# Performance work log

Measured on AMD Instinct MI355X. Metric: run time of the kernel, lower is better.

The kernel has to match this reference:

```python
import jax, jax.numpy as jnp
import numpy as np


def setup_inputs() -> dict:
    key = jax.random.key(0)
    k1, k2, k3, k4, k5 = jax.random.split(key, 5)
    N, C, H, W, HID = 32, 3, 64, 64, 256
    x = jax.random.normal(k1, (N, C, H, W), dtype=jnp.float32)
    w_xh = jax.random.normal(k2, (HID, C), dtype=jnp.float32) * (1.0 / np.sqrt(C))
    b_xh = jax.random.normal(k3, (HID,), dtype=jnp.float32) * 0.02
    w_hh = jax.random.normal(k4, (HID, HID), dtype=jnp.float32) * (1.0 / np.sqrt(HID))
    b_hh = jax.random.normal(k5, (HID,), dtype=jnp.float32) * 0.02
    return {"x": x, "w_xh": w_xh, "b_xh": b_xh, "w_hh": w_hh, "b_hh": b_hh}


def reference(x, w_xh, b_xh, w_hh, b_hh):
    N, C, H, W = x.shape
    HID = w_hh.shape[0]
    # 1x1 convs as einsums
    xh = jnp.einsum('nchw,oc->nohw', x, w_xh) + b_xh[None, :, None, None]
    # h=None -> zeros; fc_hh(zeros) = bias broadcast
    h0 = jnp.broadcast_to(b_hh[None, :, None, None], xh.shape).astype(xh.dtype)
    # shifted neighbor views (zero-padded)
    hl = jnp.pad(h0, ((0, 0), (0, 0), (0, 0), (1, 0)))[..., :-1]   # left neighbor
    hr = jnp.pad(h0, ((0, 0), (0, 0), (0, 0), (0, 1)))[..., 1:]    # right neighbor
    ht = jnp.pad(h0, ((0, 0), (0, 0), (1, 0), (0, 0)))[:, :, :-1]  # top neighbor
    cols_even = (jnp.arange(W) % 2 == 0)
    h = jnp.where(cols_even[None, None, None, :], hl, hr) + ht
    nl = jnp.pad(xh, ((0, 0), (0, 0), (0, 0), (1, 0)))[..., :-1]
    nr = jnp.pad(xh, ((0, 0), (0, 0), (0, 0), (0, 1)))[..., 1:]
    nt = jnp.pad(xh, ((0, 0), (0, 0), (1, 0), (0, 0)))[:, :, :-1]
    nb = jnp.pad(xh, ((0, 0), (0, 0), (0, 1), (0, 0)))[:, :, 1:]
    n = nl + nr + nt + nb
    logit = jnp.transpose(h + n, (2, 3, 0, 1))  # [H, W, N, HID]

    col_idx = jnp.arange(W)

    def col_step(h_prev, xs):
        l_j, j = xs                                 # l_j: [N, HID]
        contrib = h_prev @ w_hh.T + b_hh            # F.linear
        l = l_j + jnp.where(j == 0, 0.0, 1.0) * contrib
        h_new = jax.nn.sigmoid(l)
        return h_new, h_new

    def row_step(h_below, xs):
        l_row, k = xs                               # l_row: [W, N, HID], k=0 is bottom row
        i = H - 1 - k
        below = jnp.einsum('wnh,gh->wng', h_below, w_hh) + b_hh
        l_row = l_row + jnp.where(k == 0, 0.0, 1.0) * below
        flip = (i % 2 == 0)                         # even rows scanned right-to-left
        l_dir = jnp.where(flip, l_row[::-1], l_row)
        _, h_dir = jax.lax.scan(col_step, jnp.zeros((N, HID), l_row.dtype), (l_dir, col_idx))
        h_row = jnp.where(flip, h_dir[::-1], h_dir)
        return h_row, h_row

    logit_btm_up = logit[::-1]                      # rows processed bottom-up
    _, rows = jax.lax.scan(row_step, jnp.zeros((W, N, HID), logit.dtype),
                           (logit_btm_up, jnp.arange(H)))
    h_next = rows[::-1]                             # [H, W, N, HID] in row order
    return jnp.transpose(h_next, (2, 3, 0, 1))      # [N, HID, H, W]
```

## Files before the change

### kernel.cpp

```cpp
#include <hip/hip_runtime.h>

#define HID 256
#define HH  64
#define WW  64

typedef _Float16 f16x8 __attribute__((ext_vector_type(8)));
typedef float    f32x4 __attribute__((ext_vector_type(4)));

#define LDS_BARRIER() do {                                   \
    asm volatile("s_waitcnt lgkmcnt(0)" ::: "memory");       \
    __builtin_amdgcn_sched_barrier(0);                       \
    __builtin_amdgcn_s_barrier();                            \
    __builtin_amdgcn_sched_barrier(0);                       \
  } while (0)

__global__ __launch_bounds__(256, 1)
void mrf_scan_kernel(const float* __restrict__ x,
                     const float* __restrict__ w_xh,
                     const float* __restrict__ b_xh,
                     const float* __restrict__ w_hh,
                     const float* __restrict__ b_hh,
                     float* __restrict__ out)
{
    const int n   = blockIdx.x;
    const int tid = threadIdx.x;
    const int wv  = tid >> 6;
    const int l   = tid & 63;
    const int l15 = l & 15;
    const int lq  = l >> 4;
    const int nbase = wv * 64;
    const int o   = nbase + l;

    __shared__ __align__(16) _Float16 hbel[WW][HID];
    __shared__ __align__(16) _Float16 hsum[2][HID];
    __shared__ __align__(16) float4   xs4[WW];

    {
        unsigned int* z = (unsigned int*)(&hbel[0][0]);
        #pragma unroll
        for (int q = 0; q < (WW*HID/2)/256; ++q) z[tid + 256*q] = 0u;
        ((unsigned int*)(&hsum[0][0]))[tid] = 0u;
    }

    f16x8 Bf[4][8];
    #pragma unroll
    for (int nt = 0; nt < 4; ++nt) {
        const float* wr = w_hh + (size_t)(nbase + nt*16 + l15) * HID;
        #pragma unroll
        for (int kf = 0; kf < 8; ++kf) {
            const int g0 = kf*32 + lq*8;
            f16x8 b;
            #pragma unroll
            for (int j = 0; j < 8; ++j) b[j] = (_Float16)wr[g0 + j];
            Bf[nt][kf] = b;
        }
    }

    const float wx0 = w_xh[o*3+0];
    const float wx1 = w_xh[o*3+1];
    const float wx2 = w_xh[o*3+2];
    const float bx  = b_xh[o];
    const float bh  = b_hh[o];

    const int    XP = HH*WW;
    const float* xn = x + (size_t)n * 3 * XP;
    float*     outn = out + (size_t)n * HID * XP;

    __syncthreads();

    int cur = 0;
    for (int k = 0; k < HH; ++k) {
        const int i    = HH - 1 - k;
        const int flip = ((i & 1) == 0);

        if (tid < 192) {
            const int c = tid >> 6, w = tid & 63;
            const float* xc = xn + (size_t)c * XP;
            float s = 0.f;
            if (w > 0)    s += xc[i*WW + w - 1];
            if (w < WW-1) s += xc[i*WW + w + 1];
            if (i > 0)    s += xc[(i-1)*WW + w];
            if (i < HH-1) s += xc[(i+1)*WW + w];
            ((float*)&xs4[w])[c] = s;
            if (c == 0) {
                const float cnt = (float)((w>0) + (w<WW-1) + (i>0) + (i<HH-1));
                ((float*)&xs4[w])[3] = cnt;
            }
        }
        LDS_BARRIER();

        const float Fr = ((i != 0) ? 1.f : 0.f) + ((k != 0) ? 1.f : 0.f);
        float* outrow = outn + (size_t)i * WW;

        for (int t = 0; t < WW; ++t) {
            const int w  = flip ? (WW-1-t) : t;
            const int wn = (t < WW-1) ? (flip ? (WW-2-t) : (t+1)) : w;

            f16x8 Af[8];
            #pragma unroll
            for (int kf = 0; kf < 8; ++kf)
                Af[kf] = *(const f16x8*)((const char*)(&hsum[cur][0]) + kf*64 + lq*16);
            const _Float16 hb = hbel[wn][o];
            const float4   xv = xs4[w];

            const float Ft = Fr + ((t != 0 && t != WW-1) ? 1.f : 0.f) + ((t != 0) ? 1.f : 0.f);
            float pre = xv.w * bx;
            pre = fmaf(xv.x, wx0, pre);
            pre = fmaf(xv.y, wx1, pre);
            pre = fmaf(xv.z, wx2, pre);
            pre = fmaf(Ft,   bh,  pre);

            f32x4 cA[4], cB[4];
            #pragma unroll
            for (int nt = 0; nt < 4; ++nt) {
                cA[nt] = (f32x4){0.f,0.f,0.f,0.f};
                cB[nt] = (f32x4){0.f,0.f,0.f,0.f};
            }
            #pragma unroll
            for (int nt = 0; nt < 4; ++nt) {
                #pragma unroll
                for (int kf = 0; kf < 4; ++kf) {
                    cA[nt] = __builtin_amdgcn_mfma_f32_16x16x32_f16(Af[kf],   Bf[nt][kf],   cA[nt], 0, 0, 0);
                    cB[nt] = __builtin_amdgcn_mfma_f32_16x16x32_f16(Af[kf+4], Bf[nt][kf+4], cB[nt], 0, 0, 0);
                }
            }

            const float dA = (lq < 2) ? ((lq == 0) ? cA[0][0] : cA[1][0])
                                      : ((lq == 2) ? cA[2][0] : cA[3][0]);
            const float dB = (lq < 2) ? ((lq == 0) ? cB[0][0] : cB[1][0])
                                      : ((lq == 2) ? cB[2][0] : cB[3][0]);
            const float val = dA + dB + pre;
            const float e   = __expf(-val);
            const float s   = __builtin_amdgcn_rcpf(1.f + e);

            const _Float16 h16 = (_Float16)s;
            hbel[w][o] = h16;
            hsum[cur ^ 1][o] = (t < WW-1) ? (_Float16)(h16 + hb) : h16;

            outrow[(size_t)o * XP + w] = s;

            LDS_BARRIER();
            cur ^= 1;
        }
    }
}

extern "C" void kernel_launch(void* const* d_in, const int* in_sizes, int n_in,
                              void* d_out, int out_size, void* d_ws, size_t ws_size,
                              hipStream_t stream) {
    const float* x    = (const float*)d_in[0];
    const float* w_xh = (const float*)d_in[1];
    const float* b_xh = (const float*)d_in[2];
    const float* w_hh = (const float*)d_in[3];
    const float* b_hh = (const float*)d_in[4];
    float* out = (float*)d_out;
    (void)in_sizes; (void)n_in; (void)d_ws; (void)ws_size; (void)out_size;

    mrf_scan_kernel<<<dim3(32), dim3(256), 0, stream>>>(x, w_xh, b_xh, w_hh, b_hh, out);
}
```

Baseline: 1.932 ms.

## Spread recurrent matvec over 16 waves and defer row-below and output stores

Each block now runs 1024 threads (16 waves), and each wave computes one 16-column N-tile of the per-step 256x256 f16 MFMA matvec, so the per-wave serial MFMA chain drops from 32 to 8. The pointwise sigmoid is computed only by the first quad of lanes. The writes to the below-row LDS buffer and to global output are deferred to the start of the next step, moving them off the path before the barrier. In exchange, each per-column barrier now synchronises 16 waves instead of 4, and most lanes sit idle during the pointwise work.

```diff
diff --git a/kernel.cpp b/kernel.cpp
--- a/kernel.cpp
+++ b/kernel.cpp
@@ -14,7 +14,7 @@
     __builtin_amdgcn_sched_barrier(0);                       \
   } while (0)
 
-__global__ __launch_bounds__(256, 1)
+__global__ __launch_bounds__(1024, 4)
 void mrf_scan_kernel(const float* __restrict__ x,
                      const float* __restrict__ w_xh,
                      const float* __restrict__ b_xh,
@@ -28,8 +28,7 @@
     const int l   = tid & 63;
     const int l15 = l & 15;
     const int lq  = l >> 4;
-    const int nbase = wv * 64;
-    const int o   = nbase + l;
+    const int oc  = wv * 16 + l15;
 
     __shared__ __align__(16) _Float16 hbel[WW][HID];
     __shared__ __align__(16) _Float16 hsum[2][HID];
@@ -38,37 +37,42 @@
     {
         unsigned int* z = (unsigned int*)(&hbel[0][0]);
         #pragma unroll
-        for (int q = 0; q < (WW*HID/2)/256; ++q) z[tid + 256*q] = 0u;
-        ((unsigned int*)(&hsum[0][0]))[tid] = 0u;
+        for (int q = 0; q < (WW*HID/2)/1024; ++q) z[tid + 1024*q] = 0u;
+        if (tid < 256) ((unsigned int*)(&hsum[0][0]))[tid] = 0u;
     }
 
-    f16x8 Bf[4][8];
-    #pragma unroll
-    for (int nt = 0; nt < 4; ++nt) {
-        const float* wr = w_hh + (size_t)(nbase + nt*16 + l15) * HID;
+    f16x8 Bf[8];
+    {
+        const float* wr = w_hh + (size_t)oc * HID;
         #pragma unroll
         for (int kf = 0; kf < 8; ++kf) {
             const int g0 = kf*32 + lq*8;
             f16x8 b;
             #pragma unroll
             for (int j = 0; j < 8; ++j) b[j] = (_Float16)wr[g0 + j];
-            Bf[nt][kf] = b;
+            Bf[kf] = b;
         }
     }
 
-    const float wx0 = w_xh[o*3+0];
-    const float wx1 = w_xh[o*3+1];
-    const float wx2 = w_xh[o*3+2];
-    const float bx  = b_xh[o];
-    const float bh  = b_hh[o];
+    const float wx0 = w_xh[oc*3+0];
+    const float wx1 = w_xh[oc*3+1];
+    const float wx2 = w_xh[oc*3+2];
+    const float bx  = b_xh[oc];
+    const float bh  = b_hh[oc];
 
     const int    XP = HH*WW;
     const float* xn = x + (size_t)n * 3 * XP;
-    float*     outn = out + (size_t)n * HID * XP;
+    float* outc = out + (size_t)n * HID * XP + (size_t)oc * XP;
 
     __syncthreads();
 
     int cur = 0;
+    bool     pend = false;
+    float    s_pend = 0.f;
+    _Float16 h16_pend = (_Float16)0.f;
+    float*   optr_pend = outc;
+    _Float16* hbptr_pend = &hbel[0][0];
+
     for (int k = 0; k < HH; ++k) {
         const int i    = HH - 1 - k;
         const int flip = ((i & 1) == 0);
@@ -90,59 +94,62 @@
         LDS_BARRIER();
 
         const float Fr = ((i != 0) ? 1.f : 0.f) + ((k != 0) ? 1.f : 0.f);
-        float* outrow = outn + (size_t)i * WW;
+        float* orow = outc + (size_t)i * WW;
 
         for (int t = 0; t < WW; ++t) {
             const int w  = flip ? (WW-1-t) : t;
             const int wn = (t < WW-1) ? (flip ? (WW-2-t) : (t+1)) : w;
 
+            if (pend && lq == 0) {
+                *hbptr_pend = h16_pend;
+                *optr_pend  = s_pend;
+            }
+
             f16x8 Af[8];
             #pragma unroll
             for (int kf = 0; kf < 8; ++kf)
                 Af[kf] = *(const f16x8*)((const char*)(&hsum[cur][0]) + kf*64 + lq*16);
-            const _Float16 hb = hbel[wn][o];
-            const float4   xv = xs4[w];
 
-            const float Ft = Fr + ((t != 0 && t != WW-1) ? 1.f : 0.f) + ((t != 0) ? 1.f : 0.f);
-            float pre = xv.w * bx;
-            pre = fmaf(xv.x, wx0, pre);
-            pre = fmaf(xv.y, wx1, pre);
-            pre = fmaf(xv.z, wx2, pre);
-            pre = fmaf(Ft,   bh,  pre);
+            _Float16 hb = (_Float16)0.f;
+            if (lq == 0) hb = hbel[wn][oc];
 
-            f32x4 cA[4], cB[4];
+            f32x4 cA = (f32x4){0.f,0.f,0.f,0.f};
+            f32x4 cB = (f32x4){0.f,0.f,0.f,0.f};
             #pragma unroll
-            for (int nt = 0; nt < 4; ++nt) {
-                cA[nt] = (f32x4){0.f,0.f,0.f,0.f};
-                cB[nt] = (f32x4){0.f,0.f,0.f,0.f};
-            }
-            #pragma unroll
-            for (int nt = 0; nt < 4; ++nt) {
-                #pragma unroll
-                for (int kf = 0; kf < 4; ++kf) {
-                    cA[nt] = __builtin_amdgcn_mfma_f32_16x16x32_f16(Af[kf],   Bf[nt][kf],   cA[nt], 0, 0, 0);
-                    cB[nt] = __builtin_amdgcn_mfma_f32_16x16x32_f16(Af[kf+4], Bf[nt][kf+4], cB[nt], 0, 0, 0);
-                }
+            for (int kf = 0; kf < 4; ++kf) {
+                cA = __builtin_amdgcn_mfma_f32_16x16x32_f16(Af[kf],   Bf[kf],   cA, 0, 0, 0);
+                cB = __builtin_amdgcn_mfma_f32_16x16x32_f16(Af[kf+4], Bf[kf+4], cB, 0, 0, 0);
             }
 
-            const float dA = (lq < 2) ? ((lq == 0) ? cA[0][0] : cA[1][0])
-                                      : ((lq == 2) ? cA[2][0] : cA[3][0]);
-            const float dB = (lq < 2) ? ((lq == 0) ? cB[0][0] : cB[1][0])
-                                      : ((lq == 2) ? cB[2][0] : cB[3][0]);
-            const float val = dA + dB + pre;
-            const float e   = __expf(-val);
-            const float s   = __builtin_amdgcn_rcpf(1.f + e);
+            float s = 0.f; _Float16 h16 = (_Float16)0.f;
+            if (lq == 0) {
+                const float4 xv = xs4[w];
+                const float Ft = Fr + ((t != 0 && t != WW-1) ? 1.f : 0.f)
+                                    + ((t != 0) ? 1.f : 0.f);
+                float pre = xv.w * bx;
+                pre = fmaf(xv.x, wx0, pre);
+                pre = fmaf(xv.y, wx1, pre);
+                pre = fmaf(xv.z, wx2, pre);
+                pre = fmaf(Ft,   bh,  pre);
 
-            const _Float16 h16 = (_Float16)s;
-            hbel[w][o] = h16;
-            hsum[cur ^ 1][o] = (t < WW-1) ? (_Float16)(h16 + hb) : h16;
-
-            outrow[(size_t)o * XP + w] = s;
+                const float val = cA[0] + cB[0] + pre;
+                const float e   = __expf(-val);
+                s   = __builtin_amdgcn_rcpf(1.f + e);
+                h16 = (_Float16)s;
+                hsum[cur ^ 1][oc] = (t < WW-1) ? (_Float16)(h16 + hb) : h16;
+            }
 
             LDS_BARRIER();
+
+            pend = true;
+            s_pend = s; h16_pend = h16;
+            hbptr_pend = &hbel[w][oc];
+            optr_pend  = orow + w;
             cur ^= 1;
         }
     }
+
+    if (lq == 0) *optr_pend = s_pend;
 }
 
 extern "C" void kernel_launch(void* const* d_in, const int* in_sizes, int n_in,
@@ -156,5 +163,5 @@
     float* out = (float*)d_out;
     (void)in_sizes; (void)n_in; (void)d_ws; (void)ws_size; (void)out_size;
 
-    mrf_scan_kernel<<<dim3(32), dim3(256), 0, stream>>>(x, w_xh, b_xh, w_hh, b_hh, out);
+    mrf_scan_kernel<<<dim3(32), dim3(1024), 0, stream>>>(x, w_xh, b_xh, w_hh, b_hh, out);
 }
```

Measured after the change: 2.289 ms. +18.5%, slower.
